# Performance work log

Measured on AMD Instinct MI355X. Metric: run time of the kernel, lower is better.

Reference implementation:

```python
import jax, jax.numpy as jnp
import numpy as np

E = 8      # num_traits / experts
D = 1024   # input_size per trait
H = 2048   # hidden width (hidden_sizes = [2048, 2048] -> one hidden Linear)
O = 1024   # output_size
B = 4096   # batch
TOP_K = 2


def setup_inputs() -> dict:
    key = jax.random.key(0)
    ks = jax.random.split(key, E + 8)
    s = 0.02
    inp = {f"x{i}": jax.random.normal(ks[i], (B, D), dtype=jnp.float32) for i in range(E)}
    inp["gate_w"] = jax.random.normal(ks[E + 0], (E * D, E), dtype=jnp.float32) * s
    inp["gate_b"] = jnp.zeros((E,), dtype=jnp.float32)
    inp["w_in"]  = jax.random.normal(ks[E + 1], (E, D, H), dtype=jnp.float32) * s
    inp["b_in"]  = jnp.zeros((E, H), dtype=jnp.float32)
    inp["w_h"]   = jax.random.normal(ks[E + 2], (E, H, H), dtype=jnp.float32) * s
    inp["b_h"]   = jnp.zeros((E, H), dtype=jnp.float32)
    inp["w_out"] = jax.random.normal(ks[E + 3], (E, H, O), dtype=jnp.float32) * s
    inp["b_out"] = jnp.zeros((E, O), dtype=jnp.float32)
    return inp


def reference(x0, x1, x2, x3, x4, x5, x6, x7,
              gate_w, gate_b, w_in, b_in, w_h, b_h, w_out, b_out):
    xs_list = [x0, x1, x2, x3, x4, x5, x6, x7]
    xs = jnp.stack(xs_list, axis=0)                       # [E, B, D]
    combined = jnp.concatenate(xs_list, axis=1)           # [B, E*D]

    # gating: top-2 + softmax over selected logits, scattered to dense [B, E]
    gate_logits = combined @ gate_w + gate_b              # [B, E]
    topk_vals, topk_idx = jax.lax.top_k(gate_logits, TOP_K)
    topk_w = jax.nn.softmax(topk_vals, axis=1)
    bsz = gate_logits.shape[0]
    rows = jnp.arange(bsz)[:, None]
    dense_w = jnp.zeros_like(gate_logits).at[rows, topk_idx].set(topk_w)  # [B, E]

    # per-expert MLP (dropout inactive at inference; use_skip=False).
    # Computed densely for all tokens; unselected tokens get weight 0 in the
    # combine, matching the masked dispatch/scatter math exactly.
    h = jax.nn.relu(jnp.einsum('ebd,edh->ebh', xs, w_in) + b_in[:, None, :])   # [E, B, H]
    h = jax.nn.relu(jnp.einsum('ebh,ehk->ebk', h, w_h) + b_h[:, None, :])      # [E, B, H]
    expert_out = jnp.einsum('ebk,eko->ebo', h, w_out) + b_out[:, None, :]      # [E, B, O]

    # weighted combine: sum_e dense_w[b,e] * expert_out[e,b,:]
    moe_output = jnp.einsum('ebo,be->bo', expert_out, dense_w)                 # [B, O]
    return moe_output
```

## Files before the change

kernel.cpp:

```cpp
#include <hip/hip_runtime.h>
#include <stdint.h>

#define E_ 8
#define D_ 1024
#define H_ 2048
#define O_ 1024
#define B_ 4096
#define GTOT (B_ * 2)
#define GPAD (GTOT + 128)
#define MT_MAX 16

typedef __attribute__((ext_vector_type(8))) __bf16 bf16x8;
typedef __attribute__((ext_vector_type(4))) float f32x4;
typedef unsigned short u16;
typedef __attribute__((ext_vector_type(4))) u16 u16x4;
typedef __attribute__((ext_vector_type(8))) u16 u16x8;

__device__ __forceinline__ u16 f2bf(float f) {
    union { float f; uint32_t u; } v; v.f = f;
    uint32_t u = v.u;
    return (u16)((u + 0x7FFFu + ((u >> 16) & 1u)) >> 16);
}

__device__ __forceinline__ void gl2lds16(const void* g, void* lds) {
    __builtin_amdgcn_global_load_lds(
        (__attribute__((address_space(1))) void*)(uintptr_t)g,
        (__attribute__((address_space(3))) void*)(uint32_t)(uintptr_t)lds,
        16, 0, 0);
}

struct XPtrs { const float* p[8]; };

__device__ __forceinline__ void gate_finish(int b, const double* acc, const float* __restrict__ gb,
                                            int* __restrict__ t2i, float* __restrict__ t2w) {
    float lg[8];
#pragma unroll
    for (int e = 0; e < 8; ++e) lg[e] = (float)acc[e] + gb[e];
    int i0 = 0;
#pragma unroll
    for (int e = 1; e < 8; ++e) if (lg[e] > lg[i0]) i0 = e;
    int i1 = -1;
#pragma unroll
    for (int e = 0; e < 8; ++e) {
        if (e == i0) continue;
        if (i1 < 0 || lg[e] > lg[i1]) i1 = e;
    }
    float ex = expf(lg[i1] - lg[i0]);
    float w0 = 1.0f / (1.0f + ex);
    t2i[b * 2 + 0] = i0; t2i[b * 2 + 1] = i1;
    t2w[b * 2 + 0] = w0; t2w[b * 2 + 1] = ex * w0;
}

__global__ void __launch_bounds__(256) gate_kernel(XPtrs xs, const float* __restrict__ gw,
                                                   const float* __restrict__ gb,
                                                   int* __restrict__ t2i, float* __restrict__ t2w) {
    int wave = threadIdx.x >> 6;
    int lane = threadIdx.x & 63;
    int b0 = blockIdx.x * 8 + wave * 2;
    double acc0[8], acc1[8];
#pragma unroll
    for (int e = 0; e < 8; ++e) { acc0[e] = 0.0; acc1[e] = 0.0; }
    for (int ep = 0; ep < 8; ++ep) {
        const float* xr0 = xs.p[ep] + (size_t)b0 * D_;
        const float* xr1 = xr0 + D_;
        for (int t = 0; t < D_ / 64; ++t) {
            int d = t * 64 + lane;
            float v0 = xr0[d];
            float v1 = xr1[d];
            const float* g = gw + ((size_t)(ep * D_ + d)) * 8;
#pragma unroll
            for (int e = 0; e < 8; ++e) {
                double ge = (double)g[e];
                acc0[e] += (double)v0 * ge;
                acc1[e] += (double)v1 * ge;
            }
        }
    }
#pragma unroll
    for (int e = 0; e < 8; ++e) {
        for (int off = 32; off > 0; off >>= 1) {
            acc0[e] += __shfl_xor(acc0[e], off, 64);
            acc1[e] += __shfl_xor(acc1[e], off, 64);
        }
    }
    if (lane == 0) {
        gate_finish(b0 + 0, acc0, gb, t2i, t2w);
        gate_finish(b0 + 1, acc1, gb, t2i, t2w);
    }
}

__global__ void __launch_bounds__(256) route_build(const int* __restrict__ t2i,
                                                   int* __restrict__ offs, int* __restrict__ cursor) {
    __shared__ int cnt[8];
    int t = threadIdx.x;
    if (t < 8) cnt[t] = 0;
    __syncthreads();
    for (int i = t; i < B_ * 2; i += 256) atomicAdd(&cnt[t2i[i]], 1);
    __syncthreads();
    if (t == 0) {
        int run = 0;
        for (int e = 0; e < 8; ++e) { offs[e] = run; cursor[e] = run; run += cnt[e]; }
        offs[8] = run;
    }
}

__global__ void __launch_bounds__(256) scatter_gather(XPtrs xs, const int* __restrict__ t2i,
                                                      int* __restrict__ cursor, int* __restrict__ slot,
                                                      u16* __restrict__ A1) {
    int b = blockIdx.x;
    int t = threadIdx.x;
    __shared__ int gsh[2];
    int e0 = t2i[b * 2 + 0], e1 = t2i[b * 2 + 1];
    if (t == 0) {
        int g0 = atomicAdd(&cursor[e0], 1);
        int g1 = atomicAdd(&cursor[e1], 1);
        gsh[0] = g0; gsh[1] = g1;
        slot[b * 2 + 0] = g0; slot[b * 2 + 1] = g1;
    }
    __syncthreads();
    int g0 = gsh[0], g1 = gsh[1];
    float4 v0 = ((const float4*)(xs.p[e0] + (size_t)b * D_))[t];
    float4 v1 = ((const float4*)(xs.p[e1] + (size_t)b * D_))[t];
    u16x4 o0, o1;
    o0.x = f2bf(v0.x); o0.y = f2bf(v0.y); o0.z = f2bf(v0.z); o0.w = f2bf(v0.w);
    o1.x = f2bf(v1.x); o1.y = f2bf(v1.y); o1.z = f2bf(v1.z); o1.w = f2bf(v1.w);
    ((u16x4*)(A1 + (size_t)g0 * D_))[t] = o0;
    ((u16x4*)(A1 + (size_t)g1 * D_))[t] = o1;
}

__global__ void __launch_bounds__(256) wconv(const float* __restrict__ w, u16* __restrict__ wt,
                                             int K, int N) {
    __shared__ float tile[64][33];
    int e = blockIdx.z;
    int n0 = blockIdx.x * 32, k0 = blockIdx.y * 64;
    int tid = threadIdx.x;
    int tx = tid & 31, ty = tid >> 5;
    const float* wp = w + (size_t)e * K * N + (size_t)k0 * N + n0;
#pragma unroll
    for (int r = 0; r < 8; ++r)
        tile[ty + r * 8][tx] = wp[(size_t)(ty + r * 8) * N + tx];
    __syncthreads();
    int n = tid >> 3, kq = tid & 7;
    u16x8 o;
#pragma unroll
    for (int i = 0; i < 8; ++i) o[i] = f2bf(tile[kq * 8 + i][n]);
    u16* op = wt + (size_t)e * N * K + (size_t)(n0 + n) * K + k0 + kq * 8;
    *(u16x8*)op = o;
}

__global__ void __launch_bounds__(256) expert_gemm(const u16* __restrict__ A, const u16* __restrict__ Wt,
                                                   const float* __restrict__ bias,
                                                   u16* __restrict__ outB, float* __restrict__ outF,
                                                   const int* __restrict__ offs, int K, int N, int relu) {
    int bid = blockIdx.x;
    int e = bid & 7;
    int j = bid >> 3;
    int mt = j & (MT_MAX - 1);
    int nt = j >> 4;
    int row0 = offs[e];
    int cnt = offs[e + 1] - row0;
    if (mt * 128 >= cnt) return;

    __shared__ __align__(16) u16 sA[3][128 * 32];
    __shared__ __align__(16) u16 sB[3][128 * 32];

    int tid = threadIdx.x;
    int wave = tid >> 6, lane = tid & 63;
    int wm = wave & 1, wn = wave >> 1;
    int l15 = lane & 15, quad = lane >> 4;
    int rsub = lane >> 2;
    int koff = (((lane & 3) ^ (rsub & 3) ^ ((rsub >> 2) & 3)) * 8);
    int physOff = (quad ^ (l15 & 3) ^ ((l15 >> 2) & 3)) * 8;

    f32x4 acc[4][4];
#pragma unroll
    for (int i = 0; i < 4; ++i)
#pragma unroll
        for (int jj = 0; jj < 4; ++jj) acc[i][jj] = (f32x4){0.f, 0.f, 0.f, 0.f};

    const u16* Abase = A + (size_t)(row0 + mt * 128) * K;
    const u16* Bbase = Wt + ((size_t)e * N + (size_t)nt * 128) * K;

    int kSteps = K / 32;

    auto issue = [&](int ks, int bufIdx) {
        int k0 = ks * 32;
        u16* dA = &sA[bufIdx][0];
        u16* dB = &sB[bufIdx][0];
#pragma unroll
        for (int c = 0; c < 2; ++c) {
            int ch = wave * 2 + c;
            int r = ch * 16 + rsub;
            gl2lds16(Abase + (size_t)r * K + k0 + koff, dA + ch * 512);
            gl2lds16(Bbase + (size_t)r * K + k0 + koff, dB + ch * 512);
        }
    };

    issue(0, 0);
    issue(1, 1);
    int bc = 0, bi = 2;
    for (int ks = 0; ks < kSteps; ++ks) {
        if (ks + 1 < kSteps) __builtin_amdgcn_s_waitcnt(0x74);
        else                 __builtin_amdgcn_s_waitcnt(0x70);
        __builtin_amdgcn_s_barrier();
        if (ks + 2 < kSteps) issue(ks + 2, bi);

        const u16* a_ = &sA[bc][0];
        const u16* b_ = &sB[bc][0];
        bf16x8 af[4], bfr[4];
#pragma unroll
        for (int tm = 0; tm < 4; ++tm) {
            int row = wm * 64 + tm * 16 + l15;
            af[tm] = *(const bf16x8*)(a_ + row * 32 + physOff);
        }
#pragma unroll
        for (int tn = 0; tn < 4; ++tn) {
            int row = wn * 64 + tn * 16 + l15;
            bfr[tn] = *(const bf16x8*)(b_ + row * 32 + physOff);
        }
        __builtin_amdgcn_s_setprio(1);
#pragma unroll
        for (int tm = 0; tm < 4; ++tm)
#pragma unroll
            for (int tn = 0; tn < 4; ++tn)
                acc[tm][tn] = __builtin_amdgcn_mfma_f32_16x16x32_bf16(af[tm], bfr[tn], acc[tm][tn], 0, 0, 0);
        __builtin_amdgcn_s_setprio(0);

        bc = (bc == 2) ? 0 : bc + 1;
        bi = (bi == 2) ? 0 : bi + 1;
    }

    size_t gm0 = (size_t)row0 + (size_t)mt * 128 + (size_t)wm * 64;
    int lm0 = mt * 128 + wm * 64;
    int n0 = nt * 128 + wn * 64;
#pragma unroll
    for (int tn = 0; tn < 4; ++tn) {
        int col = n0 + tn * 16 + l15;
        float bv = bias[e * N + col];
#pragma unroll
        for (int tm = 0; tm < 4; ++tm) {
#pragma unroll
            for (int r = 0; r < 4; ++r) {
                int rr = tm * 16 + quad * 4 + r;
                if (lm0 + rr < cnt) {
                    float v = acc[tm][tn][r] + bv;
                    if (relu) v = fmaxf(v, 0.f);
                    if (outB) outB[(gm0 + rr) * N + col] = f2bf(v);
                    else      outF[(gm0 + rr) * N + col] = v;
                }
            }
        }
    }
}

__global__ void __launch_bounds__(256) combine_out(const float* __restrict__ eo, const int* __restrict__ slot,
                                                   const float* __restrict__ t2w, float* __restrict__ out) {
    int b = blockIdx.x, t = threadIdx.x;
    int g0 = slot[b * 2 + 0], g1 = slot[b * 2 + 1];
    float w0 = t2w[b * 2 + 0], w1 = t2w[b * 2 + 1];
    float4 va = ((const float4*)(eo + (size_t)g0 * O_))[t];
    float4 vc = ((const float4*)(eo + (size_t)g1 * O_))[t];
    float4 r;
    r.x = w0 * va.x + w1 * vc.x;
    r.y = w0 * va.y + w1 * vc.y;
    r.z = w0 * va.z + w1 * vc.z;
    r.w = w0 * va.w + w1 * vc.w;
    ((float4*)(out + (size_t)b * O_))[t] = r;
}

extern "C" void kernel_launch(void* const* d_in, const int* in_sizes, int n_in,
                              void* d_out, int out_size, void* d_ws, size_t ws_size,
                              hipStream_t stream) {
    (void)in_sizes; (void)n_in; (void)out_size; (void)ws_size;
    XPtrs xp;
    for (int i = 0; i < 8; ++i) xp.p[i] = (const float*)d_in[i];
    const float* gate_w = (const float*)d_in[8];
    const float* gate_b = (const float*)d_in[9];
    const float* w_in  = (const float*)d_in[10];
    const float* b_in  = (const float*)d_in[11];
    const float* w_h   = (const float*)d_in[12];
    const float* b_h   = (const float*)d_in[13];
    const float* w_out = (const float*)d_in[14];
    const float* b_out = (const float*)d_in[15];
    float* out = (float*)d_out;

    char* ws = (char*)d_ws;
    size_t off = 0;
    auto alloc = [&](size_t b) { size_t o = off; off += (b + 255) & ~(size_t)255; return o; };

    size_t t2i_o  = alloc((size_t)B_ * 2 * 4);
    size_t t2w_o  = alloc((size_t)B_ * 2 * 4);
    size_t slot_o = alloc((size_t)B_ * 2 * 4);
    size_t offs_o = alloc(16 * 4);
    size_t cur_o  = alloc(8 * 4);
    size_t A1_o   = alloc((size_t)GPAD * D_ * 2);
    size_t h1_o   = alloc((size_t)GPAD * H_ * 2);
    size_t h2_o   = alloc((size_t)GPAD * H_ * 2);
    size_t wtin_o = alloc((size_t)E_ * H_ * D_ * 2);
    size_t wth_o  = alloc((size_t)E_ * H_ * H_ * 2);
    size_t wtout_o= alloc((size_t)E_ * O_ * H_ * 2);
    size_t eo_o   = A1_o;

    int*   t2i  = (int*)(ws + t2i_o);
    float* t2w  = (float*)(ws + t2w_o);
    int*   slot = (int*)(ws + slot_o);
    int*   offs = (int*)(ws + offs_o);
    int*   cur  = (int*)(ws + cur_o);
    u16*   A1   = (u16*)(ws + A1_o);
    u16*   h1   = (u16*)(ws + h1_o);
    u16*   h2   = (u16*)(ws + h2_o);
    u16*   wtin = (u16*)(ws + wtin_o);
    u16*   wth  = (u16*)(ws + wth_o);
    u16*   wtout= (u16*)(ws + wtout_o);
    float* eo   = (float*)(ws + eo_o);

    hipLaunchKernelGGL(gate_kernel, dim3(B_ / 8), dim3(256), 0, stream, xp, gate_w, gate_b, t2i, t2w);
    hipLaunchKernelGGL(route_build, dim3(1), dim3(256), 0, stream, t2i, offs, cur);
    hipLaunchKernelGGL(scatter_gather, dim3(B_), dim3(256), 0, stream, xp, t2i, cur, slot, A1);

    hipLaunchKernelGGL(wconv, dim3(H_ / 32, D_ / 64, E_), dim3(256), 0, stream, w_in, wtin, D_, H_);
    hipLaunchKernelGGL(wconv, dim3(H_ / 32, H_ / 64, E_), dim3(256), 0, stream, w_h, wth, H_, H_);
    hipLaunchKernelGGL(wconv, dim3(O_ / 32, H_ / 64, E_), dim3(256), 0, stream, w_out, wtout, H_, O_);

    hipLaunchKernelGGL(expert_gemm, dim3(E_ * MT_MAX * (H_ / 128)), dim3(256), 0, stream,
                       A1, wtin, b_in, h1, (float*)nullptr, offs, D_, H_, 1);
    hipLaunchKernelGGL(expert_gemm, dim3(E_ * MT_MAX * (H_ / 128)), dim3(256), 0, stream,
                       h1, wth, b_h, h2, (float*)nullptr, offs, H_, H_, 1);
    hipLaunchKernelGGL(expert_gemm, dim3(E_ * MT_MAX * (O_ / 128)), dim3(256), 0, stream,
                       h2, wtout, b_out, (u16*)nullptr, eo, offs, H_, O_, 0);

    hipLaunchKernelGGL(combine_out, dim3(B_), dim3(256), 0, stream, eo, slot, t2w, out);
}
```

Measured before the change: 838.5 us.

## Add 256x256-tile 8-wave expert GEMM for first two MLP layers

Adds a new expert GEMM kernel that computes a 256x256 output tile with 512 threads and 128KB of dynamic LDS. It splits each K-tile into A and B halves and interleaves async global-to-LDS loads with four MFMA phases, separated by barriers and wave priority changes (ping-pong style). It replaces the 128x128 kernel for the input and hidden layers to get more data reuse per load. In exchange it wastes more padded rows on each expert's last M tile, allows fewer blocks per CU, and may leave a wave-quantization tail; the row padding is enlarged to cover the bigger tile.

Measured after the change: 838.9 us. No clear change (+0.0%).

```diff
diff --git a/kernel.cpp b/kernel.cpp
--- a/kernel.cpp
+++ b/kernel.cpp
@@ -7,8 +7,9 @@
 #define O_ 1024
 #define B_ 4096
 #define GTOT (B_ * 2)
-#define GPAD (GTOT + 128)
+#define GPAD (GTOT + 256)
 #define MT_MAX 16
+#define MT256 8
 
 typedef __attribute__((ext_vector_type(8))) __bf16 bf16x8;
 typedef __attribute__((ext_vector_type(4))) float f32x4;
@@ -146,6 +147,200 @@
     for (int i = 0; i < 8; ++i) o[i] = f2bf(tile[kq * 8 + i][n]);
     u16* op = wt + (size_t)e * N * K + (size_t)(n0 + n) * K + k0 + kq * 8;
     *(u16x8*)op = o;
+}
+
+__global__ void __launch_bounds__(512, 2) expert_gemm256(const u16* __restrict__ A,
+                                                         const u16* __restrict__ Wt,
+                                                         const float* __restrict__ bias,
+                                                         u16* __restrict__ outB,
+                                                         const int* __restrict__ offs,
+                                                         int K, int N) {
+    int bid = blockIdx.x;
+    int e = bid & 7;
+    int j = bid >> 3;
+    int mt = j & (MT256 - 1);
+    int nt = j >> 3;
+    int row0 = offs[e];
+    int cnt = offs[e + 1] - row0;
+    if (mt * 256 >= cnt) return;
+
+    extern __shared__ __align__(16) u16 smem[];
+    u16* sA = smem;
+    u16* sB = smem + 32768;
+
+    int tid = threadIdx.x;
+    int wave = tid >> 6, lane = tid & 63;
+    int wm = wave >> 2;
+    int wn = wave & 3;
+    int l15 = lane & 15, quad = lane >> 4;
+    int swz = l15 & 7;
+
+    const u16* Abase = A + (size_t)(row0 + mt * 256) * K;
+    const u16* Bbase = Wt + ((size_t)e * N + (size_t)nt * 256) * K;
+    int NT = K >> 6;
+
+    auto stageA = [&](int tile, int half) {
+        if (tile < NT) {
+            u16* dst = sA + (((tile & 1) * 2 + half) << 13);
+            const u16* gs = Abase + (size_t)(half * 128) * K + tile * 64;
+#pragma unroll
+            for (int rr = 0; rr < 2; ++rr) {
+                int liB = rr * 512 + wave * 64;
+                int li = liB + lane;
+                int r = li >> 3;
+                int lc = (li & 7) ^ (r & 7);
+                gl2lds16(gs + (size_t)r * K + lc * 8, dst + liB * 8);
+            }
+        }
+    };
+    auto stageB = [&](int tile, int half) {
+        if (tile < NT) {
+            u16* dst = sB + (((tile & 1) * 2 + half) << 13);
+            const u16* gs = Bbase + (size_t)(half * 128) * K + tile * 64;
+#pragma unroll
+            for (int rr = 0; rr < 2; ++rr) {
+                int liB = rr * 512 + wave * 64;
+                int li = liB + lane;
+                int r = li >> 3;
+                int lc = (li & 7) ^ (r & 7);
+                gl2lds16(gs + (size_t)r * K + lc * 8, dst + liB * 8);
+            }
+        }
+    };
+
+    f32x4 acc[2][2][4][2];
+#pragma unroll
+    for (int a = 0; a < 2; ++a)
+#pragma unroll
+        for (int b = 0; b < 2; ++b)
+#pragma unroll
+            for (int c = 0; c < 4; ++c)
+#pragma unroll
+                for (int dd = 0; dd < 2; ++dd) acc[a][b][c][dd] = (f32x4){0.f, 0.f, 0.f, 0.f};
+
+    stageA(0, 0); stageB(0, 0); stageA(0, 1); stageB(0, 1);
+    stageA(1, 0); stageB(1, 0);
+    __builtin_amdgcn_s_waitcnt(0x74);
+    __builtin_amdgcn_s_barrier();
+
+    bf16x8 af[4][2];
+    bf16x8 bfr[2][2][2];
+
+    for (int T = 0; T < NT; ++T) {
+        int d = T & 1;
+        const u16* aB0 = sA + ((d * 2 + 0) << 13);
+        const u16* aB1 = sA + ((d * 2 + 1) << 13);
+        const u16* bB0 = sB + ((d * 2 + 0) << 13);
+        const u16* bB1 = sB + ((d * 2 + 1) << 13);
+
+#pragma unroll
+        for (int fm = 0; fm < 4; ++fm) {
+            int rh = wm * 64 + fm * 16 + l15;
+#pragma unroll
+            for (int kc = 0; kc < 2; ++kc)
+                af[fm][kc] = *(const bf16x8*)(aB0 + rh * 64 + (((kc << 2) | quad) ^ swz) * 8);
+        }
+#pragma unroll
+        for (int fn = 0; fn < 2; ++fn) {
+            int rh = wn * 32 + fn * 16 + l15;
+#pragma unroll
+            for (int kc = 0; kc < 2; ++kc)
+                bfr[0][fn][kc] = *(const bf16x8*)(bB0 + rh * 64 + (((kc << 2) | quad) ^ swz) * 8);
+        }
+        stageA(T + 1, 1);
+        __builtin_amdgcn_s_barrier();
+        __builtin_amdgcn_s_setprio(1);
+#pragma unroll
+        for (int fm = 0; fm < 4; ++fm)
+#pragma unroll
+            for (int fn = 0; fn < 2; ++fn)
+#pragma unroll
+                for (int kc = 0; kc < 2; ++kc)
+                    acc[0][0][fm][fn] = __builtin_amdgcn_mfma_f32_16x16x32_bf16(
+                        af[fm][kc], bfr[0][fn][kc], acc[0][0][fm][fn], 0, 0, 0);
+        __builtin_amdgcn_s_setprio(0);
+        __builtin_amdgcn_s_barrier();
+
+#pragma unroll
+        for (int fn = 0; fn < 2; ++fn) {
+            int rh = wn * 32 + fn * 16 + l15;
+#pragma unroll
+            for (int kc = 0; kc < 2; ++kc)
+                bfr[1][fn][kc] = *(const bf16x8*)(bB1 + rh * 64 + (((kc << 2) | quad) ^ swz) * 8);
+        }
+        stageB(T + 1, 1);
+        __builtin_amdgcn_s_barrier();
+        __builtin_amdgcn_s_setprio(1);
+#pragma unroll
+        for (int fm = 0; fm < 4; ++fm)
+#pragma unroll
+            for (int fn = 0; fn < 2; ++fn)
+#pragma unroll
+                for (int kc = 0; kc < 2; ++kc)
+                    acc[0][1][fm][fn] = __builtin_amdgcn_mfma_f32_16x16x32_bf16(
+                        af[fm][kc], bfr[1][fn][kc], acc[0][1][fm][fn], 0, 0, 0);
+        __builtin_amdgcn_s_setprio(0);
+        __builtin_amdgcn_s_barrier();
+
+#pragma unroll
+        for (int fm = 0; fm < 4; ++fm) {
+            int rh = wm * 64 + fm * 16 + l15;
+#pragma unroll
+            for (int kc = 0; kc < 2; ++kc)
+                af[fm][kc] = *(const bf16x8*)(aB1 + rh * 64 + (((kc << 2) | quad) ^ swz) * 8);
+        }
+        stageA(T + 2, 0);
+        __builtin_amdgcn_s_barrier();
+        __builtin_amdgcn_s_setprio(1);
+#pragma unroll
+        for (int fm = 0; fm < 4; ++fm)
+#pragma unroll
+            for (int fn = 0; fn < 2; ++fn)
+#pragma unroll
+                for (int kc = 0; kc < 2; ++kc)
+                    acc[1][0][fm][fn] = __builtin_amdgcn_mfma_f32_16x16x32_bf16(
+                        af[fm][kc], bfr[0][fn][kc], acc[1][0][fm][fn], 0, 0, 0);
+        __builtin_amdgcn_s_setprio(0);
+        __builtin_amdgcn_s_barrier();
+
+        stageB(T + 2, 0);
+        __builtin_amdgcn_s_barrier();
+        __builtin_amdgcn_s_setprio(1);
+#pragma unroll
+        for (int fm = 0; fm < 4; ++fm)
+#pragma unroll
+            for (int fn = 0; fn < 2; ++fn)
+#pragma unroll
+                for (int kc = 0; kc < 2; ++kc)
+                    acc[1][1][fm][fn] = __builtin_amdgcn_mfma_f32_16x16x32_bf16(
+                        af[fm][kc], bfr[1][fn][kc], acc[1][1][fm][fn], 0, 0, 0);
+        __builtin_amdgcn_s_setprio(0);
+        if (T + 2 < NT) __builtin_amdgcn_s_waitcnt(0x74);
+        else            __builtin_amdgcn_s_waitcnt(0x70);
+        __builtin_amdgcn_s_barrier();
+    }
+
+#pragma unroll
+    for (int mh = 0; mh < 2; ++mh)
+#pragma unroll
+        for (int nh = 0; nh < 2; ++nh)
+#pragma unroll
+            for (int fn = 0; fn < 2; ++fn) {
+                int col = nt * 256 + nh * 128 + wn * 32 + fn * 16 + l15;
+                float bv = bias[e * N + col];
+#pragma unroll
+                for (int fm = 0; fm < 4; ++fm) {
+                    int rloc = mt * 256 + mh * 128 + wm * 64 + fm * 16 + quad * 4;
+#pragma unroll
+                    for (int r = 0; r < 4; ++r) {
+                        if (rloc + r < cnt) {
+                            float v = acc[mh][nh][fm][fn][r] + bv;
+                            v = fmaxf(v, 0.f);
+                            outB[(size_t)(row0 + rloc + r) * N + col] = f2bf(v);
+                        }
+                    }
+                }
+            }
 }
 
 __global__ void __launch_bounds__(256) expert_gemm(const u16* __restrict__ A, const u16* __restrict__ Wt,
@@ -272,6 +467,14 @@
                               void* d_out, int out_size, void* d_ws, size_t ws_size,
                               hipStream_t stream) {
     (void)in_sizes; (void)n_in; (void)out_size; (void)ws_size;
+
+    static bool lds_attr_set = false;
+    if (!lds_attr_set) {
+        hipFuncSetAttribute((const void*)expert_gemm256,
+                            hipFuncAttributeMaxDynamicSharedMemorySize, 131072);
+        lds_attr_set = true;
+    }
+
     XPtrs xp;
     for (int i = 0; i < 8; ++i) xp.p[i] = (const float*)d_in[i];
     const float* gate_w = (const float*)d_in[8];
@@ -322,10 +525,10 @@
     hipLaunchKernelGGL(wconv, dim3(H_ / 32, H_ / 64, E_), dim3(256), 0, stream, w_h, wth, H_, H_);
     hipLaunchKernelGGL(wconv, dim3(O_ / 32, H_ / 64, E_), dim3(256), 0, stream, w_out, wtout, H_, O_);
 
-    hipLaunchKernelGGL(expert_gemm, dim3(E_ * MT_MAX * (H_ / 128)), dim3(256), 0, stream,
-                       A1, wtin, b_in, h1, (float*)nullptr, offs, D_, H_, 1);
-    hipLaunchKernelGGL(expert_gemm, dim3(E_ * MT_MAX * (H_ / 128)), dim3(256), 0, stream,
-                       h1, wth, b_h, h2, (float*)nullptr, offs, H_, H_, 1);
+    hipLaunchKernelGGL(expert_gemm256, dim3(E_ * MT256 * (H_ / 256)), dim3(512), 131072, stream,
+                       A1, wtin, b_in, h1, offs, D_, H_);
+    hipLaunchKernelGGL(expert_gemm256, dim3(E_ * MT256 * (H_ / 256)), dim3(512), 131072, stream,
+                       h1, wth, b_h, h2, offs, H_, H_);
     hipLaunchKernelGGL(expert_gemm, dim3(E_ * MT_MAX * (O_ / 128)), dim3(256), 0, stream,
                        h2, wtout, b_out, (u16*)nullptr, eo, offs, H_, O_, 0);
 
```
